# Performance work log

Measured on AMD Instinct MI355X. Metric: run time of the kernel, lower is better.

## Reference

```python
import jax, jax.numpy as jnp
import numpy as np
import math

D_MODEL = 512
N_HEADS = 8
D_K = D_MODEL // N_HEADS
B, S = 2, 4096
LN_EPS = 1e-5


def _xavier(key, fan_in, fan_out):
    limit = math.sqrt(6.0 / (fan_in + fan_out))
    return jax.random.uniform(key, (fan_in, fan_out), jnp.float32, -limit, limit)


def setup_inputs() -> dict:
    key = jax.random.key(0)
    ks = jax.random.split(key, 12)
    x = jax.random.normal(ks[0], (B, S, D_MODEL), jnp.float32)
    consciousness_state = jax.random.normal(ks[1], (B, D_MODEL), jnp.float32)
    # weights stored as [in, out] (equivalent to torch Linear weight.T)
    w_q = _xavier(ks[2], D_MODEL, D_MODEL)
    w_k = _xavier(ks[3], D_MODEL, D_MODEL)
    w_v = _xavier(ks[4], D_MODEL, D_MODEL)
    w_o = _xavier(ks[5], D_MODEL, D_MODEL)
    b_o = jnp.zeros((D_MODEL,), jnp.float32)
    w_gate = _xavier(ks[6], D_MODEL, N_HEADS)
    b_gate = jnp.zeros((N_HEADS,), jnp.float32)
    w_int = _xavier(ks[7], D_MODEL, D_MODEL)
    b_int = jnp.zeros((D_MODEL,), jnp.float32)
    ln_gamma = jnp.ones((D_MODEL,), jnp.float32)
    ln_beta = jnp.zeros((D_MODEL,), jnp.float32)
    return {"x": x, "consciousness_state": consciousness_state,
            "w_q": w_q, "w_k": w_k, "w_v": w_v, "w_o": w_o, "b_o": b_o,
            "w_gate": w_gate, "b_gate": b_gate, "w_int": w_int, "b_int": b_int,
            "ln_gamma": ln_gamma, "ln_beta": ln_beta}


def reference(x, consciousness_state, w_q, w_k, w_v, w_o, b_o,
              w_gate, b_gate, w_int, b_int, ln_gamma, ln_beta):
    b, s, d = x.shape
    # project and split heads: [B, H, S, d_k]
    def heads(w):
        return (x @ w).reshape(b, s, N_HEADS, D_K).transpose(0, 2, 1, 3)
    Q, K, V = heads(w_q), heads(w_k), heads(w_v)
    scores = jnp.einsum('bhsd,bhtd->bhst', Q, K) / math.sqrt(D_K)  # [B,H,S,S]
    # per-head consciousness gate BEFORE softmax
    cw = jax.nn.sigmoid(consciousness_state @ w_gate + b_gate)  # [B,H]
    scores = scores * cw[:, :, None, None]
    attn = jax.nn.softmax(scores, axis=-1)
    # dropout is identity in eval mode
    context = jnp.einsum('bhst,bhtd->bhsd', attn, V)
    context = context.transpose(0, 2, 1, 3).reshape(b, s, d)
    out = context @ w_o + b_o
    iw = jax.nn.sigmoid(consciousness_state @ w_int + b_int)  # [B,D]
    out = out * iw[:, None, :]
    # residual + LayerNorm
    h = out + x
    mu = jnp.mean(h, axis=-1, keepdims=True)
    var = jnp.var(h, axis=-1, keepdims=True)
    out = (h - mu) * jax.lax.rsqrt(var + LN_EPS) * ln_gamma + ln_beta
    return out, attn.mean(axis=1)
```

## Files before the change

kernel.cpp:

```cpp
#include <hip/hip_runtime.h>
#include <hip/hip_bf16.h>

using short8 = __attribute__((ext_vector_type(8))) short;
using f32x4  = __attribute__((ext_vector_type(4))) float;

#define S_LEN 4096
#define DM 512

__device__ __forceinline__ unsigned short f2b(float f) {
    unsigned int u = __float_as_uint(f);
    u += 0x7fffu + ((u >> 16) & 1u);
    return (unsigned short)(u >> 16);
}

__device__ __forceinline__ short8 pack8(float4 a, float4 b) {
    short8 r;
    r[0] = (short)f2b(a.x); r[1] = (short)f2b(a.y); r[2] = (short)f2b(a.z); r[3] = (short)f2b(a.w);
    r[4] = (short)f2b(b.x); r[5] = (short)f2b(b.y); r[6] = (short)f2b(b.z); r[7] = (short)f2b(b.w);
    return r;
}

__global__ __launch_bounds__(256) void convert_w(
    const float* __restrict__ w0, const float* __restrict__ w1,
    const float* __restrict__ w2, const float* __restrict__ w3,
    unsigned short* __restrict__ t0, unsigned short* __restrict__ t1,
    unsigned short* __restrict__ t2, unsigned short* __restrict__ t3)
{
    __shared__ float sh[64][65];
    const float* src; unsigned short* dst;
    switch (blockIdx.z) {
        case 0: src = w0; dst = t0; break;
        case 1: src = w1; dst = t1; break;
        case 2: src = w2; dst = t2; break;
        default: src = w3; dst = t3; break;
    }
    int k0 = blockIdx.x * 64, n0 = blockIdx.y * 64;
    int tid = threadIdx.x;
    for (int i = tid; i < 4096; i += 256) {
        int k = i >> 6, n = i & 63;
        sh[k][n] = src[(size_t)(k0 + k) * DM + n0 + n];
    }
    __syncthreads();
    for (int i = tid; i < 4096; i += 256) {
        int n = i >> 6, k = i & 63;
        dst[(size_t)(n0 + n) * DM + k0 + k] = f2b(sh[k][n]);
    }
}

__global__ __launch_bounds__(256) void convert_x(
    const float* __restrict__ x, unsigned short* __restrict__ xb)
{
    size_t i = ((size_t)blockIdx.x * 256 + threadIdx.x) * 8;
    float4 a = *reinterpret_cast<const float4*>(x + i);
    float4 b = *reinterpret_cast<const float4*>(x + i + 4);
    *reinterpret_cast<short8*>(xb + i) = pack8(a, b);
}

__global__ __launch_bounds__(64) void gates_kernel(
    const float* __restrict__ cs, const float* __restrict__ wg, const float* __restrict__ bg,
    const float* __restrict__ wi, const float* __restrict__ bi,
    float* __restrict__ cwout, float* __restrict__ iwout)
{
    int o = blockIdx.x, b = blockIdx.y, lane = threadIdx.x;
    const float* c = cs + (size_t)b * DM;
    float acc = 0.f;
    if (o < 8) {
        #pragma unroll
        for (int j = 0; j < 8; ++j) { int k = j * 64 + lane; acc += c[k] * wg[(size_t)k * 8 + o]; }
    } else {
        int n = o - 8;
        #pragma unroll
        for (int j = 0; j < 8; ++j) { int k = j * 64 + lane; acc += c[k] * wi[(size_t)k * DM + n]; }
    }
    #pragma unroll
    for (int d = 32; d; d >>= 1) acc += __shfl_xor(acc, d);
    if (lane == 0) {
        if (o < 8) cwout[b * 8 + o] = 1.f / (1.f + __expf(-(acc + bg[o])));
        else       iwout[b * DM + (o - 8)] = 1.f / (1.f + __expf(-(acc + bi[o - 8])));
    }
}

__global__ __launch_bounds__(256) void gemm_qkv(
    const unsigned short* __restrict__ A, const unsigned short* __restrict__ WT,
    const float* __restrict__ cw,
    unsigned short* __restrict__ Qb, unsigned short* __restrict__ Kb,
    unsigned short* __restrict__ Vt)
{
    __shared__ unsigned short a_sh[64][72];
    __shared__ unsigned short b_sh[64][72];
    const int m0 = blockIdx.x * 64;
    const int n0g = blockIdx.y * 64;
    const int which = blockIdx.y >> 3;
    const int tid = threadIdx.x;
    const int wave = tid >> 6, lane = tid & 63;
    const int g = lane >> 4, lr = lane & 15;
    const int srow = tid >> 3, skc = (tid & 7) * 8;

    float sq = 1.f;
    if (which == 0) {
        int b = blockIdx.x >> 6;
        int h = blockIdx.y & 7;
        sq = cw[b * 8 + h] * 0.125f * 1.44269504f;
    }

    f32x4 acc[4];
    #pragma unroll
    for (int i = 0; i < 4; ++i) acc[i] = (f32x4){0.f, 0.f, 0.f, 0.f};

    short8 ar[2], br[2];
    #pragma unroll
    for (int cc = 0; cc < 2; ++cc) {
        int row = srow + cc * 32;
        ar[cc] = *reinterpret_cast<const short8*>(A  + (size_t)(m0  + row) * DM + skc);
        br[cc] = *reinterpret_cast<const short8*>(WT + (size_t)(n0g + row) * DM + skc);
    }

    for (int k0 = 0; k0 < 512; k0 += 64) {
        #pragma unroll
        for (int cc = 0; cc < 2; ++cc) {
            int row = srow + cc * 32;
            *reinterpret_cast<short8*>(&a_sh[row][skc]) = ar[cc];
            *reinterpret_cast<short8*>(&b_sh[row][skc]) = br[cc];
        }
        __syncthreads();
        if (k0 + 64 < 512) {
            #pragma unroll
            for (int cc = 0; cc < 2; ++cc) {
                int row = srow + cc * 32;
                ar[cc] = *reinterpret_cast<const short8*>(A  + (size_t)(m0  + row) * DM + k0 + 64 + skc);
                br[cc] = *reinterpret_cast<const short8*>(WT + (size_t)(n0g + row) * DM + k0 + 64 + skc);
            }
        }
        __builtin_amdgcn_s_setprio(1);
        #pragma unroll
        for (int ks = 0; ks < 2; ++ks) {
            short8 af = *reinterpret_cast<const short8*>(&a_sh[wave * 16 + lr][ks * 32 + g * 8]);
            #pragma unroll
            for (int nf = 0; nf < 4; ++nf) {
                short8 bf = *reinterpret_cast<const short8*>(&b_sh[nf * 16 + lr][ks * 32 + g * 8]);
                acc[nf] = __builtin_amdgcn_mfma_f32_16x16x32_bf16(af, bf, acc[nf], 0, 0, 0);
            }
        }
        __builtin_amdgcn_s_setprio(0);
        __syncthreads();
    }

    #pragma unroll
    for (int nf = 0; nf < 4; ++nf) {
        #pragma unroll
        for (int r = 0; r < 4; ++r) {
            int m = m0 + wave * 16 + g * 4 + r;
            int nl = (blockIdx.y & 7) * 64 + nf * 16 + lr;
            unsigned short v = f2b(acc[nf][r] * sq);
            if (which == 0) {
                Qb[(size_t)m * DM + nl] = v;
            } else if (which == 1) {
                Kb[(size_t)m * DM + nl] = v;
            } else {
                int b = m >> 12, s = m & 4095;
                int h = nl >> 6, d = nl & 63;
                Vt[((size_t)(b * 8 + h) * 64 + d) * S_LEN + s] = v;
            }
        }
    }
}

__global__ __launch_bounds__(256) void gemm_proj(
    const unsigned short* __restrict__ A, const unsigned short* __restrict__ WT,
    float* __restrict__ outf, const float* __restrict__ bias,
    const float* __restrict__ iw, const float* __restrict__ xres)
{
    __shared__ unsigned short a_sh[64][72];
    __shared__ unsigned short b_sh[64][72];
    const int m0 = blockIdx.x * 64;
    const int n0 = blockIdx.y * 64;
    const int tid = threadIdx.x;
    const int wave = tid >> 6, lane = tid & 63;
    const int g = lane >> 4, lr = lane & 15;
    const int srow = tid >> 3, skc = (tid & 7) * 8;

    f32x4 acc[4];
    #pragma unroll
    for (int i = 0; i < 4; ++i) acc[i] = (f32x4){0.f, 0.f, 0.f, 0.f};

    short8 ar[2], br[2];
    #pragma unroll
    for (int cc = 0; cc < 2; ++cc) {
        int row = srow + cc * 32;
        ar[cc] = *reinterpret_cast<const short8*>(A  + (size_t)(m0 + row) * DM + skc);
        br[cc] = *reinterpret_cast<const short8*>(WT + (size_t)(n0 + row) * DM + skc);
    }

    for (int k0 = 0; k0 < 512; k0 += 64) {
        #pragma unroll
        for (int cc = 0; cc < 2; ++cc) {
            int row = srow + cc * 32;
            *reinterpret_cast<short8*>(&a_sh[row][skc]) = ar[cc];
            *reinterpret_cast<short8*>(&b_sh[row][skc]) = br[cc];
        }
        __syncthreads();
        if (k0 + 64 < 512) {
            #pragma unroll
            for (int cc = 0; cc < 2; ++cc) {
                int row = srow + cc * 32;
                ar[cc] = *reinterpret_cast<const short8*>(A  + (size_t)(m0 + row) * DM + k0 + 64 + skc);
                br[cc] = *reinterpret_cast<const short8*>(WT + (size_t)(n0 + row) * DM + k0 + 64 + skc);
            }
        }
        __builtin_amdgcn_s_setprio(1);
        #pragma unroll
        for (int ks = 0; ks < 2; ++ks) {
            short8 af = *reinterpret_cast<const short8*>(&a_sh[wave * 16 + lr][ks * 32 + g * 8]);
            #pragma unroll
            for (int nf = 0; nf < 4; ++nf) {
                short8 bf = *reinterpret_cast<const short8*>(&b_sh[nf * 16 + lr][ks * 32 + g * 8]);
                acc[nf] = __builtin_amdgcn_mfma_f32_16x16x32_bf16(af, bf, acc[nf], 0, 0, 0);
            }
        }
        __builtin_amdgcn_s_setprio(0);
        __syncthreads();
    }

    #pragma unroll
    for (int nf = 0; nf < 4; ++nf) {
        #pragma unroll
        for (int r = 0; r < 4; ++r) {
            int m = m0 + wave * 16 + g * 4 + r;
            int n = n0 + nf * 16 + lr;
            int b = m >> 12;
            float v = (acc[nf][r] + bias[n]) * iw[b * DM + n] + xres[(size_t)m * DM + n];
            outf[(size_t)m * DM + n] = v;
        }
    }
}

__global__ __launch_bounds__(256) void attn_ctx(
    const unsigned short* __restrict__ Qb, const unsigned short* __restrict__ Kb,
    const unsigned short* __restrict__ Vt,
    float* __restrict__ lbuf, unsigned short* __restrict__ ctx)
{
    __shared__ unsigned short k_sh[64][72];
    __shared__ unsigned short v_sh[64][72];
    __shared__ unsigned short p_sh[4][16][72];
    const int q0 = blockIdx.x * 64;
    const int bh = blockIdx.y;
    const int b = bh >> 3, h = bh & 7;
    const int tid = threadIdx.x, wave = tid >> 6, lane = tid & 63;
    const int g = lane >> 4, lr = lane & 15;
    const int srow = tid >> 3, skc = (tid & 7) * 8;

    short8 qf[2];
    {
        const unsigned short* qp = Qb + (size_t)(b * S_LEN + q0 + wave * 16 + lr) * DM + h * 64;
        qf[0] = *reinterpret_cast<const short8*>(qp + g * 8);
        qf[1] = *reinterpret_cast<const short8*>(qp + 32 + g * 8);
    }
    short8 onesb;
    #pragma unroll
    for (int i = 0; i < 8; ++i) onesb[i] = (short)0x3F80;

    f32x4 lsum = (f32x4){0.f, 0.f, 0.f, 0.f};
    f32x4 cacc[4];
    #pragma unroll
    for (int i = 0; i < 4; ++i) cacc[i] = (f32x4){0.f, 0.f, 0.f, 0.f};

    const unsigned short* Kbase = Kb + (size_t)(b * S_LEN) * DM + h * 64;
    const unsigned short* Vbase = Vt + ((size_t)bh * 64) * S_LEN;

    short8 kr[2], vr[2];
    #pragma unroll
    for (int cc = 0; cc < 2; ++cc) {
        int row = srow + cc * 32;
        kr[cc] = *reinterpret_cast<const short8*>(Kbase + (size_t)row * DM + skc);
        vr[cc] = *reinterpret_cast<const short8*>(Vbase + (size_t)row * S_LEN + skc);
    }

    for (int kv0 = 0; kv0 < S_LEN; kv0 += 64) {
        #pragma unroll
        for (int cc = 0; cc < 2; ++cc) {
            int row = srow + cc * 32;
            *reinterpret_cast<short8*>(&k_sh[row][skc]) = kr[cc];
            *reinterpret_cast<short8*>(&v_sh[row][skc]) = vr[cc];
        }
        __syncthreads();
        f32x4 st[4];
        #pragma unroll
        for (int f = 0; f < 4; ++f) st[f] = (f32x4){0.f, 0.f, 0.f, 0.f};
        __builtin_amdgcn_s_setprio(1);
        #pragma unroll
        for (int ks = 0; ks < 2; ++ks) {
            #pragma unroll
            for (int f = 0; f < 4; ++f) {
                short8 kf = *reinterpret_cast<const short8*>(&k_sh[f * 16 + lr][ks * 32 + g * 8]);
                st[f] = __builtin_amdgcn_mfma_f32_16x16x32_bf16(kf, qf[ks], st[f], 0, 0, 0);
            }
        }
        __builtin_amdgcn_s_setprio(0);
        if (kv0 + 64 < S_LEN) {
            #pragma unroll
            for (int cc = 0; cc < 2; ++cc) {
                int row = srow + cc * 32;
                kr[cc] = *reinterpret_cast<const short8*>(Kbase + (size_t)(kv0 + 64 + row) * DM + skc);
                vr[cc] = *reinterpret_cast<const short8*>(Vbase + (size_t)row * S_LEN + kv0 + 64 + skc);
            }
        }
        #pragma unroll
        for (int f = 0; f < 4; ++f) {
            float p0 = __builtin_amdgcn_exp2f(st[f][0]);
            float p1 = __builtin_amdgcn_exp2f(st[f][1]);
            float p2 = __builtin_amdgcn_exp2f(st[f][2]);
            float p3 = __builtin_amdgcn_exp2f(st[f][3]);
            unsigned u0, u1;
            asm("v_cvt_pk_bf16_f32 %0, %1, %2" : "=v"(u0) : "v"(p0), "v"(p1));
            asm("v_cvt_pk_bf16_f32 %0, %1, %2" : "=v"(u1) : "v"(p2), "v"(p3));
            uint2 pv; pv.x = u0; pv.y = u1;
            *reinterpret_cast<uint2*>(&p_sh[wave][lr][f * 16 + g * 4]) = pv;
        }
        __builtin_amdgcn_s_setprio(1);
        #pragma unroll
        for (int ks = 0; ks < 2; ++ks) {
            short8 pf = *reinterpret_cast<const short8*>(&p_sh[wave][lr][ks * 32 + g * 8]);
            lsum = __builtin_amdgcn_mfma_f32_16x16x32_bf16(pf, onesb, lsum, 0, 0, 0);
            #pragma unroll
            for (int df = 0; df < 4; ++df) {
                short8 vf = *reinterpret_cast<const short8*>(&v_sh[df * 16 + lr][ks * 32 + g * 8]);
                cacc[df] = __builtin_amdgcn_mfma_f32_16x16x32_bf16(pf, vf, cacc[df], 0, 0, 0);
            }
        }
        __builtin_amdgcn_s_setprio(0);
        __syncthreads();
    }
    float rl[4];
    #pragma unroll
    for (int r = 0; r < 4; ++r) rl[r] = 1.f / lsum[r];
    if (lr == 0) {
        #pragma unroll
        for (int r = 0; r < 4; ++r)
            lbuf[bh * S_LEN + q0 + wave * 16 + g * 4 + r] = lsum[r];
    }
    #pragma unroll
    for (int df = 0; df < 4; ++df) {
        #pragma unroll
        for (int r = 0; r < 4; ++r) {
            int q = q0 + wave * 16 + g * 4 + r;
            ctx[(size_t)(b * S_LEN + q) * DM + h * 64 + df * 16 + lr] = f2b(cacc[df][r] * rl[r]);
        }
    }
}

__global__ __launch_bounds__(256) void attn_mean(
    const unsigned short* __restrict__ Qb, const unsigned short* __restrict__ Kb,
    const float* __restrict__ lbuf, float* __restrict__ outmean)
{
    __shared__ unsigned short k_sh[32][520];
    const int kc0 = blockIdx.x * 512;
    const int q0 = blockIdx.y * 64;
    const int b = blockIdx.z;
    const int tid = threadIdx.x, wave = tid >> 6, lane = tid & 63;
    const int g = lane >> 4, lr = lane & 15;
    const int srow = tid >> 6, scol = (tid & 63) * 8;

    float la2[8][4];
    #pragma unroll
    for (int h = 0; h < 8; ++h) {
        #pragma unroll
        for (int r = 0; r < 4; ++r) {
            int idx = (b * 8 + h) * S_LEN + q0 + wave * 16 + g * 4 + r;
            la2[h][r] = -log2f(lbuf[idx]) - 3.0f;
        }
    }
    const unsigned short* qbase = Qb + (size_t)(b * S_LEN + q0 + wave * 16 + lr) * DM;
    const unsigned short* Kbase = Kb + (size_t)(b * S_LEN) * DM;

    short8 stg[8];
    #pragma unroll
    for (int i = 0; i < 8; ++i) {
        int row = srow + i * 4;
        stg[i] = *reinterpret_cast<const short8*>(Kbase + (size_t)(kc0 + row) * DM + scol);
    }

    for (int t = 0; t < 16; ++t) {
        int kv0 = kc0 + t * 32;
        #pragma unroll
        for (int i = 0; i < 8; ++i) {
            int row = srow + i * 4;
            *reinterpret_cast<short8*>(&k_sh[row][scol]) = stg[i];
        }
        __syncthreads();
        if (t + 1 < 16) {
            #pragma unroll
            for (int i = 0; i < 8; ++i) {
                int row = srow + i * 4;
                stg[i] = *reinterpret_cast<const short8*>(Kbase + (size_t)(kv0 + 32 + row) * DM + scol);
            }
        }
        float macc[2][4];
        #pragma unroll
        for (int f = 0; f < 2; ++f)
            #pragma unroll
            for (int r = 0; r < 4; ++r) macc[f][r] = 0.f;
        #pragma unroll
        for (int h = 0; h < 8; ++h) {
            const unsigned short* qp = qbase + h * 64;
            short8 qf0 = *reinterpret_cast<const short8*>(qp + g * 8);
            short8 qf1 = *reinterpret_cast<const short8*>(qp + 32 + g * 8);
            f32x4 s[2];
            s[0] = (f32x4){0.f, 0.f, 0.f, 0.f};
            s[1] = (f32x4){0.f, 0.f, 0.f, 0.f};
            __builtin_amdgcn_s_setprio(1);
            #pragma unroll
            for (int f = 0; f < 2; ++f) {
                short8 kf0 = *reinterpret_cast<const short8*>(&k_sh[f * 16 + lr][h * 64 + g * 8]);
                s[f] = __builtin_amdgcn_mfma_f32_16x16x32_bf16(qf0, kf0, s[f], 0, 0, 0);
                short8 kf1 = *reinterpret_cast<const short8*>(&k_sh[f * 16 + lr][h * 64 + 32 + g * 8]);
                s[f] = __builtin_amdgcn_mfma_f32_16x16x32_bf16(qf1, kf1, s[f], 0, 0, 0);
            }
            __builtin_amdgcn_s_setprio(0);
            #pragma unroll
            for (int f = 0; f < 2; ++f)
                #pragma unroll
                for (int r = 0; r < 4; ++r)
                    macc[f][r] += __builtin_amdgcn_exp2f(s[f][r] + la2[h][r]);
        }
        #pragma unroll
        for (int f = 0; f < 2; ++f) {
            #pragma unroll
            for (int r = 0; r < 4; ++r) {
                int q = q0 + wave * 16 + g * 4 + r;
                outmean[(size_t)(b * S_LEN + q) * S_LEN + kv0 + f * 16 + lr] = macc[f][r];
            }
        }
        __syncthreads();
    }
}

__global__ __launch_bounds__(64) void ln_kernel(
    const float* __restrict__ hbuf, const float* __restrict__ gamma,
    const float* __restrict__ beta, float* __restrict__ dout)
{
    int row = blockIdx.x, lane = threadIdx.x;
    const float* hp = hbuf + (size_t)row * DM + lane * 8;
    float4 v0 = *reinterpret_cast<const float4*>(hp);
    float4 v1 = *reinterpret_cast<const float4*>(hp + 4);
    float s = v0.x + v0.y + v0.z + v0.w + v1.x + v1.y + v1.z + v1.w;
    float ss = v0.x * v0.x + v0.y * v0.y + v0.z * v0.z + v0.w * v0.w
             + v1.x * v1.x + v1.y * v1.y + v1.z * v1.z + v1.w * v1.w;
    #pragma unroll
    for (int d = 32; d; d >>= 1) { s += __shfl_xor(s, d); ss += __shfl_xor(ss, d); }
    float mu = s * (1.f / 512.f);
    float var = ss * (1.f / 512.f) - mu * mu;
    float rstd = rsqrtf(var + 1e-5f);
    float4 g0 = *reinterpret_cast<const float4*>(gamma + lane * 8);
    float4 g1 = *reinterpret_cast<const float4*>(gamma + lane * 8 + 4);
    float4 b0 = *reinterpret_cast<const float4*>(beta + lane * 8);
    float4 b1 = *reinterpret_cast<const float4*>(beta + lane * 8 + 4);
    float4 o0, o1;
    o0.x = (v0.x - mu) * rstd * g0.x + b0.x;
    o0.y = (v0.y - mu) * rstd * g0.y + b0.y;
    o0.z = (v0.z - mu) * rstd * g0.z + b0.z;
    o0.w = (v0.w - mu) * rstd * g0.w + b0.w;
    o1.x = (v1.x - mu) * rstd * g1.x + b1.x;
    o1.y = (v1.y - mu) * rstd * g1.y + b1.y;
    o1.z = (v1.z - mu) * rstd * g1.z + b1.z;
    o1.w = (v1.w - mu) * rstd * g1.w + b1.w;
    float* op = dout + (size_t)row * DM + lane * 8;
    *reinterpret_cast<float4*>(op) = o0;
    *reinterpret_cast<float4*>(op + 4) = o1;
}

extern "C" void kernel_launch(void* const* d_in, const int* in_sizes, int n_in,
                              void* d_out, int out_size, void* d_ws, size_t ws_size,
                              hipStream_t stream)
{
    const float* x   = (const float*)d_in[0];
    const float* cs  = (const float*)d_in[1];
    const float* wq  = (const float*)d_in[2];
    const float* wk  = (const float*)d_in[3];
    const float* wv  = (const float*)d_in[4];
    const float* wo  = (const float*)d_in[5];
    const float* bo  = (const float*)d_in[6];
    const float* wg  = (const float*)d_in[7];
    const float* bg  = (const float*)d_in[8];
    const float* wi  = (const float*)d_in[9];
    const float* bi  = (const float*)d_in[10];
    const float* gam = (const float*)d_in[11];
    const float* bet = (const float*)d_in[12];

    float* out = (float*)d_out;
    float* outmean = out + (size_t)2 * S_LEN * DM;

    char* ws = (char*)d_ws;
    size_t off = 0;
    auto alloc = [&](size_t bytes) { void* p = ws + off; off += (bytes + 255) & ~(size_t)255; return p; };

    unsigned short* wtq = (unsigned short*)alloc((size_t)DM * DM * 2);
    unsigned short* wtk = (unsigned short*)alloc((size_t)DM * DM * 2);
    unsigned short* wtv = (unsigned short*)alloc((size_t)DM * DM * 2);
    unsigned short* wto = (unsigned short*)alloc((size_t)DM * DM * 2);
    unsigned short* xb  = (unsigned short*)alloc((size_t)2 * S_LEN * DM * 2);
    unsigned short* Qb  = (unsigned short*)alloc((size_t)2 * S_LEN * DM * 2);
    unsigned short* Kb  = (unsigned short*)alloc((size_t)2 * S_LEN * DM * 2);
    unsigned short* Vt  = (unsigned short*)alloc((size_t)2 * S_LEN * DM * 2);
    unsigned short* ctx = (unsigned short*)alloc((size_t)2 * S_LEN * DM * 2);
    float* lbuf = (float*)alloc((size_t)16 * S_LEN * 4);
    float* cwb  = (float*)alloc(64);
    float* iwb  = (float*)alloc((size_t)2 * DM * 4);
    float* hbuf = (float*)Qb;

    convert_w<<<dim3(8, 8, 4), 256, 0, stream>>>(wq, wk, wv, wo, wtq, wtk, wtv, wto);
    convert_x<<<dim3(2048), 256, 0, stream>>>(x, xb);
    gates_kernel<<<dim3(520, 2), 64, 0, stream>>>(cs, wg, bg, wi, bi, cwb, iwb);

    gemm_qkv<<<dim3(128, 24), 256, 0, stream>>>(xb, wtq, cwb, Qb, Kb, Vt);

    attn_ctx<<<dim3(64, 16), 256, 0, stream>>>(Qb, Kb, Vt, lbuf, ctx);
    attn_mean<<<dim3(8, 64, 2), 256, 0, stream>>>(Qb, Kb, lbuf, outmean);

    gemm_proj<<<dim3(128, 8), 256, 0, stream>>>(ctx, wto, hbuf, bo, iwb, x);
    ln_kernel<<<dim3(2 * S_LEN), 64, 0, stream>>>(hbuf, gam, bet, out);
}
```

Baseline: 277.4 us.

## Switch attention context kernel to 32x32 MFMA with split-KV waves and LDS reduction

Rewrites the attn_ctx inner loop to use 32x32x16 bf16 MFMA tiles instead of 16x16x32. Each wave now computes a 32-query by 32-key block, with the four waves split two ways over queries and two ways over KV halves. The partial context and row sums are merged through an LDS scratch reduction at the end. The goal is fewer LDS fragment reads and MFMA issues per tile, at the cost of more accumulator registers and an extra reduction step with a sync.

```diff
diff --git a/kernel.cpp b/kernel.cpp
--- a/kernel.cpp
+++ b/kernel.cpp
@@ -3,6 +3,7 @@
 
 using short8 = __attribute__((ext_vector_type(8))) short;
 using f32x4  = __attribute__((ext_vector_type(4))) float;
+using f32x16 = __attribute__((ext_vector_type(16))) float;
 
 #define S_LEN 4096
 #define DM 512
@@ -239,30 +240,35 @@
     const unsigned short* __restrict__ Vt,
     float* __restrict__ lbuf, unsigned short* __restrict__ ctx)
 {
-    __shared__ unsigned short k_sh[64][72];
-    __shared__ unsigned short v_sh[64][72];
-    __shared__ unsigned short p_sh[4][16][72];
+    __shared__ __align__(16) unsigned char smem[27648];
+    unsigned short (*k_sh)[72] = (unsigned short (*)[72])smem;
+    unsigned short (*v_sh)[72] = (unsigned short (*)[72])(smem + 9216);
+    unsigned short (*p_sh)[36] = (unsigned short (*)[36])(smem + 18432);
+    float* fscr = (float*)smem;
+
     const int q0 = blockIdx.x * 64;
     const int bh = blockIdx.y;
     const int b = bh >> 3, h = bh & 7;
     const int tid = threadIdx.x, wave = tid >> 6, lane = tid & 63;
-    const int g = lane >> 4, lr = lane & 15;
+    const int qh = wave & 1, kvh = wave >> 1;
+    const int l31 = lane & 31, hi = lane >> 5;
     const int srow = tid >> 3, skc = (tid & 7) * 8;
 
-    short8 qf[2];
+    short8 qf[4];
     {
-        const unsigned short* qp = Qb + (size_t)(b * S_LEN + q0 + wave * 16 + lr) * DM + h * 64;
-        qf[0] = *reinterpret_cast<const short8*>(qp + g * 8);
-        qf[1] = *reinterpret_cast<const short8*>(qp + 32 + g * 8);
+        const unsigned short* qp = Qb + (size_t)(b * S_LEN + q0 + qh * 32 + l31) * DM + h * 64 + hi * 8;
+        qf[0] = *reinterpret_cast<const short8*>(qp);
+        qf[1] = *reinterpret_cast<const short8*>(qp + 16);
+        qf[2] = *reinterpret_cast<const short8*>(qp + 32);
+        qf[3] = *reinterpret_cast<const short8*>(qp + 48);
     }
     short8 onesb;
     #pragma unroll
     for (int i = 0; i < 8; ++i) onesb[i] = (short)0x3F80;
 
-    f32x4 lsum = (f32x4){0.f, 0.f, 0.f, 0.f};
-    f32x4 cacc[4];
-    #pragma unroll
-    for (int i = 0; i < 4; ++i) cacc[i] = (f32x4){0.f, 0.f, 0.f, 0.f};
+    f32x16 lsum, cacc0, cacc1;
+    #pragma unroll
+    for (int i = 0; i < 16; ++i) { lsum[i] = 0.f; cacc0[i] = 0.f; cacc1[i] = 0.f; }
 
     const unsigned short* Kbase = Kb + (size_t)(b * S_LEN) * DM + h * 64;
     const unsigned short* Vbase = Vt + ((size_t)bh * 64) * S_LEN;
@@ -275,6 +281,8 @@
         vr[cc] = *reinterpret_cast<const short8*>(Vbase + (size_t)row * S_LEN + skc);
     }
 
+    unsigned short* prow = &p_sh[wave * 32 + l31][0];
+
     for (int kv0 = 0; kv0 < S_LEN; kv0 += 64) {
         #pragma unroll
         for (int cc = 0; cc < 2; ++cc) {
@@ -283,17 +291,14 @@
             *reinterpret_cast<short8*>(&v_sh[row][skc]) = vr[cc];
         }
         __syncthreads();
-        f32x4 st[4];
-        #pragma unroll
-        for (int f = 0; f < 4; ++f) st[f] = (f32x4){0.f, 0.f, 0.f, 0.f};
+        f32x16 st;
+        #pragma unroll
+        for (int i = 0; i < 16; ++i) st[i] = 0.f;
         __builtin_amdgcn_s_setprio(1);
         #pragma unroll
-        for (int ks = 0; ks < 2; ++ks) {
-            #pragma unroll
-            for (int f = 0; f < 4; ++f) {
-                short8 kf = *reinterpret_cast<const short8*>(&k_sh[f * 16 + lr][ks * 32 + g * 8]);
-                st[f] = __builtin_amdgcn_mfma_f32_16x16x32_bf16(kf, qf[ks], st[f], 0, 0, 0);
-            }
+        for (int kk = 0; kk < 4; ++kk) {
+            short8 kf = *reinterpret_cast<const short8*>(&k_sh[kvh * 32 + l31][kk * 16 + hi * 8]);
+            st = __builtin_amdgcn_mfma_f32_32x32x16_bf16(kf, qf[kk], st, 0, 0, 0);
         }
         __builtin_amdgcn_s_setprio(0);
         if (kv0 + 64 < S_LEN) {
@@ -305,45 +310,58 @@
             }
         }
         #pragma unroll
-        for (int f = 0; f < 4; ++f) {
-            float p0 = __builtin_amdgcn_exp2f(st[f][0]);
-            float p1 = __builtin_amdgcn_exp2f(st[f][1]);
-            float p2 = __builtin_amdgcn_exp2f(st[f][2]);
-            float p3 = __builtin_amdgcn_exp2f(st[f][3]);
+        for (int kq = 0; kq < 4; ++kq) {
+            float p0 = __builtin_amdgcn_exp2f(st[4 * kq + 0]);
+            float p1 = __builtin_amdgcn_exp2f(st[4 * kq + 1]);
+            float p2 = __builtin_amdgcn_exp2f(st[4 * kq + 2]);
+            float p3 = __builtin_amdgcn_exp2f(st[4 * kq + 3]);
             unsigned u0, u1;
             asm("v_cvt_pk_bf16_f32 %0, %1, %2" : "=v"(u0) : "v"(p0), "v"(p1));
             asm("v_cvt_pk_bf16_f32 %0, %1, %2" : "=v"(u1) : "v"(p2), "v"(p3));
             uint2 pv; pv.x = u0; pv.y = u1;
-            *reinterpret_cast<uint2*>(&p_sh[wave][lr][f * 16 + g * 4]) = pv;
+            *reinterpret_cast<uint2*>(prow + 8 * kq + 4 * hi) = pv;
         }
         __builtin_amdgcn_s_setprio(1);
         #pragma unroll
-        for (int ks = 0; ks < 2; ++ks) {
-            short8 pf = *reinterpret_cast<const short8*>(&p_sh[wave][lr][ks * 32 + g * 8]);
-            lsum = __builtin_amdgcn_mfma_f32_16x16x32_bf16(pf, onesb, lsum, 0, 0, 0);
-            #pragma unroll
-            for (int df = 0; df < 4; ++df) {
-                short8 vf = *reinterpret_cast<const short8*>(&v_sh[df * 16 + lr][ks * 32 + g * 8]);
-                cacc[df] = __builtin_amdgcn_mfma_f32_16x16x32_bf16(pf, vf, cacc[df], 0, 0, 0);
-            }
+        for (int kb = 0; kb < 2; ++kb) {
+            short8 pa = *reinterpret_cast<const short8*>(prow + kb * 16 + hi * 8);
+            lsum = __builtin_amdgcn_mfma_f32_32x32x16_bf16(pa, onesb, lsum, 0, 0, 0);
+            short8 vf0 = *reinterpret_cast<const short8*>(&v_sh[l31][kvh * 32 + kb * 16 + hi * 8]);
+            cacc0 = __builtin_amdgcn_mfma_f32_32x32x16_bf16(pa, vf0, cacc0, 0, 0, 0);
+            short8 vf1 = *reinterpret_cast<const short8*>(&v_sh[32 + l31][kvh * 32 + kb * 16 + hi * 8]);
+            cacc1 = __builtin_amdgcn_mfma_f32_32x32x16_bf16(pa, vf1, cacc1, 0, 0, 0);
         }
         __builtin_amdgcn_s_setprio(0);
         __syncthreads();
     }
-    float rl[4];
-    #pragma unroll
-    for (int r = 0; r < 4; ++r) rl[r] = 1.f / lsum[r];
-    if (lr == 0) {
-        #pragma unroll
-        for (int r = 0; r < 4; ++r)
-            lbuf[bh * S_LEN + q0 + wave * 16 + g * 4 + r] = lsum[r];
-    }
-    #pragma unroll
-    for (int df = 0; df < 4; ++df) {
-        #pragma unroll
-        for (int r = 0; r < 4; ++r) {
-            int q = q0 + wave * 16 + g * 4 + r;
-            ctx[(size_t)(b * S_LEN + q) * DM + h * 64 + df * 16 + lr] = f2b(cacc[df][r] * rl[r]);
+    float* myscr = fscr + (size_t)(qh * 64 + lane) * 52;
+    if (kvh == 1) {
+        #pragma unroll
+        for (int i = 0; i < 16; ++i) {
+            myscr[i]      = cacc0[i];
+            myscr[16 + i] = cacc1[i];
+            myscr[32 + i] = lsum[i];
+        }
+    }
+    __syncthreads();
+    if (kvh == 0) {
+        #pragma unroll
+        for (int i = 0; i < 16; ++i) {
+            cacc0[i] += myscr[i];
+            cacc1[i] += myscr[16 + i];
+            lsum[i]  += myscr[32 + i];
+        }
+        float rl[16];
+        #pragma unroll
+        for (int i = 0; i < 16; ++i) rl[i] = 1.f / lsum[i];
+        #pragma unroll
+        for (int reg = 0; reg < 16; ++reg) {
+            int row = (reg & 3) + 8 * (reg >> 2) + 4 * hi;
+            int q = q0 + qh * 32 + row;
+            unsigned short* cp = ctx + (size_t)(b * S_LEN + q) * DM + h * 64 + l31;
+            cp[0]  = f2b(cacc0[reg] * rl[reg]);
+            cp[32] = f2b(cacc1[reg] * rl[reg]);
+            if (l31 == 0) lbuf[bh * S_LEN + q] = lsum[reg];
         }
     }
 }
```

After: 307.5 us. 1.11x slower.
